# Kernel optimization log

Measured on AMD Instinct MI355X. Metric: run time of the kernel, lower is better.

Reference implementation:

```python
import jax, jax.numpy as jnp
import numpy as np

TEMPERATURE = 0.07
ALPHA = 1.0
GAMMA = 2.0
EPS = 1e-12  # F.normalize eps


def _l2_normalize(x):
    # matches F.normalize: x / max(||x||_2, eps)
    norm = jnp.sqrt(jnp.sum(x * x, axis=-1, keepdims=True))
    return x / jnp.maximum(norm, EPS)


def setup_inputs() -> dict:
    key = jax.random.key(0)
    k1, k2 = jax.random.split(key)
    B, D = 8192, 64
    image_features = jax.random.normal(k1, (B, D), dtype=jnp.float32)
    text_features = jax.random.normal(k2, (B, D), dtype=jnp.float32)
    return {"image_features": image_features, "text_features": text_features}


def reference(image_features, text_features):
    img = _l2_normalize(image_features)
    txt = _l2_normalize(text_features)
    logits = jnp.einsum("bd,cd->bc", img, txt) / TEMPERATURE  # [B, B]
    B = logits.shape[0]
    idx = jnp.arange(B)

    logp_row = jax.nn.log_softmax(logits, axis=-1)  # i2t CE source
    logp_col = jax.nn.log_softmax(logits, axis=0)   # t2i CE source

    diag_logp_row = logp_row[idx, idx]
    diag_logp_col = logp_col[idx, idx]

    # focal weight uses ROW-softmax positive prob for BOTH directions (as in source)
    p_pos = jnp.exp(diag_logp_row)
    w = ALPHA * (1.0 - p_pos) ** GAMMA

    focal_i2t = jnp.mean(w * (-diag_logp_row))
    focal_t2i = jnp.mean(w * (-diag_logp_col))
    return (focal_i2t + focal_t2i) / 2.0
```

## Files before the change

### kernel.cpp

```cpp
#include <hip/hip_runtime.h>
#include <hip/hip_bf16.h>


#define NB 8192
#define ND 64

constexpr float INV_T = 1.0f / 0.07f;
constexpr float LOG2E = 1.4426950408889634f;
constexpr float LN2   = 0.6931471805599453f;
constexpr float K1    = INV_T * LOG2E;

typedef float  floatx4 __attribute__((ext_vector_type(4)));
typedef short  bf16x8  __attribute__((ext_vector_type(8)));
typedef short  shortx4 __attribute__((ext_vector_type(4)));

__global__ __launch_bounds__(256)
void norm_kernel(const float* __restrict__ img, const float* __restrict__ txt,
                 __hip_bfloat16* __restrict__ imgB,
                 __hip_bfloat16* __restrict__ txtB,
                 float* __restrict__ diag,
                 float* __restrict__ out)
{
    if (blockIdx.x == 0 && threadIdx.x == 0) out[0] = 0.f;

    const int lane = threadIdx.x & 63;
    const int gw   = blockIdx.x * 4 + (threadIdx.x >> 6);
    const int sub  = lane >> 4;
    const int c16  = lane & 15;
    const int row  = gw * 4 + sub;

    const floatx4 x = ((const floatx4*)img)[row * 16 + c16];
    const floatx4 t = ((const floatx4*)txt)[row * 16 + c16];
    float sx  = x[0]*x[0] + x[1]*x[1] + x[2]*x[2] + x[3]*x[3];
    float st  = t[0]*t[0] + t[1]*t[1] + t[2]*t[2] + t[3]*t[3];
    float sxt = x[0]*t[0] + x[1]*t[1] + x[2]*t[2] + x[3]*t[3];
    #pragma unroll
    for (int o = 1; o < 16; o <<= 1) {
        sx  += __shfl_xor(sx,  o, 64);
        st  += __shfl_xor(st,  o, 64);
        sxt += __shfl_xor(sxt, o, 64);
    }
    const float nx = fmaxf(sqrtf(sx), 1e-12f);
    const float nt = fmaxf(sqrtf(st), 1e-12f);
    shortx4 xb, tb;
    #pragma unroll
    for (int j = 0; j < 4; ++j) {
        __hip_bfloat16 hx = __float2bfloat16(x[j] / nx * K1);
        __hip_bfloat16 ht = __float2bfloat16(t[j] / nt);
        xb[j] = *reinterpret_cast<const short*>(&hx);
        tb[j] = *reinterpret_cast<const short*>(&ht);
    }
    ((shortx4*)imgB)[row * 16 + c16] = xb;
    ((shortx4*)txtB)[row * 16 + c16] = tb;
    if (c16 == 0) diag[row] = sxt / (nx * nt) * INV_T;
}

__global__ __launch_bounds__(256)
void score_kernel(const __hip_bfloat16* __restrict__ imgB,
                  const __hip_bfloat16* __restrict__ txtB,
                  float* __restrict__ rowPart,
                  float* __restrict__ colPart)
{
    const int wid   = threadIdx.x >> 6;
    const int lane  = threadIdx.x & 63;
    const int chunk = blockIdx.x & 31;
    const int sgrp  = blockIdx.x >> 5;
    const int strip = sgrp * 4 + wid;
    const int m = lane & 15;
    const int q = lane >> 4;

    __shared__ float sm[4][256];

    const bf16x8* __restrict__ A  = (const bf16x8*)imgB;
    const bf16x8* __restrict__ Bp = (const bf16x8*)txtB;

    const int rowbase = strip * 64;
    bf16x8 a[4][2];
    #pragma unroll
    for (int it = 0; it < 4; ++it) {
        const int r = rowbase + it * 16 + m;
        a[it][0] = A[r * 8 + q];
        a[it][1] = A[r * 8 + 4 + q];
    }

    const int colbase = chunk * 256 + m;
    bf16x8 b0 = Bp[colbase * 8 + q];
    bf16x8 b1 = Bp[colbase * 8 + 4 + q];

    float rs[16];
    #pragma unroll
    for (int i = 0; i < 16; ++i) rs[i] = 0.f;

    const floatx4 NEGK = {-K1, -K1, -K1, -K1};

    #pragma unroll 2
    for (int t = 0; t < 16; ++t) {
        const int nn = colbase + (((t + 1) & 15) << 4);
        const bf16x8 pb0 = Bp[nn * 8 + q];
        const bf16x8 pb1 = Bp[nn * 8 + 4 + q];

        float csp[4];
        #pragma unroll
        for (int it = 0; it < 4; ++it) {
            floatx4 z   = __builtin_amdgcn_mfma_f32_16x16x32_bf16(a[it][0], b0, NEGK, 0, 0, 0);
            floatx4 acc = __builtin_amdgcn_mfma_f32_16x16x32_bf16(a[it][1], b1, z,    0, 0, 0);
            const float e0 = __builtin_amdgcn_exp2f(acc[0]);
            const float e1 = __builtin_amdgcn_exp2f(acc[1]);
            const float e2 = __builtin_amdgcn_exp2f(acc[2]);
            const float e3 = __builtin_amdgcn_exp2f(acc[3]);
            rs[it * 4 + 0] += e0;
            rs[it * 4 + 1] += e1;
            rs[it * 4 + 2] += e2;
            rs[it * 4 + 3] += e3;
            csp[it] = (e0 + e1) + (e2 + e3);
        }
        float cs = (csp[0] + csp[1]) + (csp[2] + csp[3]);
        cs += __shfl_xor(cs, 16, 64);
        cs += __shfl_xor(cs, 32, 64);
        if (q == 0) sm[wid][(t << 4) + m] = cs;
        b0 = pb0; b1 = pb1;
    }

#define RS_STAGE(d)                                                     \
    {                                                                   \
        const bool hi = (m & (d)) != 0;                                 \
        _Pragma("unroll")                                               \
        for (int j = 0; j < (d); ++j) {                                 \
            const float va = rs[j], vb = rs[j + (d)];                   \
            const float send = hi ? va : vb;                            \
            const float recv = __shfl_xor(send, (d), 64);               \
            rs[j] = (hi ? vb : va) + recv;                              \
        }                                                               \
    }
    RS_STAGE(8)
    RS_STAGE(4)
    RS_STAGE(2)
    RS_STAGE(1)
#undef RS_STAGE

    const int row = rowbase + ((m >> 2) << 4) + (q << 2) + (m & 3);
    rowPart[chunk * NB + row] = rs[0];

    __syncthreads();
    const int j = threadIdx.x;
    const float v = (sm[0][j] + sm[1][j]) + (sm[2][j] + sm[3][j]);
    colPart[sgrp * NB + chunk * 256 + j] = v;
}

__global__ __launch_bounds__(256)
void finish_kernel(const float* __restrict__ rowPart,
                   const float* __restrict__ colPart,
                   const float* __restrict__ diag,
                   float* __restrict__ out)
{
    const int tg = blockIdx.x * 256 + threadIdx.x;
    const int i  = tg >> 3;
    const int p  = threadIdx.x & 7;

    float rowS = 0.f, colS = 0.f;
    #pragma unroll
    for (int u = 0; u < 4; ++u) {
        rowS += rowPart[(p * 4 + u) * NB + i];
        colS += colPart[(p * 4 + u) * NB + i];
    }
    #pragma unroll
    for (int o = 1; o < 8; o <<= 1) {
        rowS += __shfl_xor(rowS, o, 64);
        colS += __shfl_xor(colS, o, 64);
    }

    float contrib = 0.f;
    if (p == 0) {
        const float d     = diag[i];
        const float lse_r = INV_T + __builtin_amdgcn_logf(rowS) * LN2;
        const float lse_c = INV_T + __builtin_amdgcn_logf(colS) * LN2;
        const float lpr = d - lse_r;
        const float lpc = d - lse_c;
        const float pp  = __builtin_amdgcn_exp2f(lpr * LOG2E);
        const float om  = 1.f - pp;
        contrib = om * om * (-lpr - lpc) * (0.5f / (float)NB);
    }
    #pragma unroll
    for (int o = 8; o < 64; o <<= 1) contrib += __shfl_xor(contrib, o, 64);

    __shared__ float red[4];
    if ((threadIdx.x & 63) == 0) red[threadIdx.x >> 6] = contrib;
    __syncthreads();
    if (threadIdx.x == 0)
        atomicAdd(out, red[0] + red[1] + red[2] + red[3]);
}

extern "C" void kernel_launch(void* const* d_in, const int* in_sizes, int n_in,
                              void* d_out, int out_size, void* d_ws, size_t ws_size,
                              hipStream_t stream)
{
    const float* img = (const float*)d_in[0];
    const float* txt = (const float*)d_in[1];

    char* ws = (char*)d_ws;
    __hip_bfloat16* imgB = (__hip_bfloat16*)(ws);
    __hip_bfloat16* txtB = (__hip_bfloat16*)(ws + (1u << 20));
    float* diag    = (float*)(ws + (2u << 20));
    float* rowPart = (float*)(ws + (2u << 20) + (1u << 15));
    float* colPart = (float*)(ws + (3u << 20) + (1u << 15));

    norm_kernel<<<512, 256, 0, stream>>>(img, txt, imgB, txtB, diag, (float*)d_out);
    score_kernel<<<1024, 256, 0, stream>>>(imgB, txtB, rowPart, colPart);
    finish_kernel<<<256, 256, 0, stream>>>(rowPart, colPart, diag, (float*)d_out);
}
```

Measured before the change: 84.71 us.

## Fuse norm, score and finish into one cooperative kernel with grid syncs

Merges the three launches into a single cooperative kernel of 1024 blocks that uses grid.sync() between the normalize, score and reduction phases. The finish phase is re-split so each of the 1024 blocks handles 8 rows, with 32 lanes per row. The aim is to remove the launch gaps and tail effects between kernels. The cost is two grid-wide barriers and a requirement that all 1024 blocks are co-resident (launch bounds 256,4); if the cooperative launch fails, the code falls back to the original three-kernel path.

```diff
diff --git a/kernel.cpp b/kernel.cpp
--- a/kernel.cpp
+++ b/kernel.cpp
@@ -1,5 +1,8 @@
 #include <hip/hip_runtime.h>
 #include <hip/hip_bf16.h>
+#include <hip/hip_cooperative_groups.h>
+
+namespace cg = cooperative_groups;
 
 
 #define NB 8192
@@ -14,20 +17,16 @@
 typedef short  bf16x8  __attribute__((ext_vector_type(8)));
 typedef short  shortx4 __attribute__((ext_vector_type(4)));
 
-__global__ __launch_bounds__(256)
-void norm_kernel(const float* __restrict__ img, const float* __restrict__ txt,
-                 __hip_bfloat16* __restrict__ imgB,
-                 __hip_bfloat16* __restrict__ txtB,
-                 float* __restrict__ diag,
-                 float* __restrict__ out)
-{
-    if (blockIdx.x == 0 && threadIdx.x == 0) out[0] = 0.f;
-
-    const int lane = threadIdx.x & 63;
-    const int gw   = blockIdx.x * 4 + (threadIdx.x >> 6);
-    const int sub  = lane >> 4;
-    const int c16  = lane & 15;
-    const int row  = gw * 4 + sub;
+__device__ __forceinline__
+void norm_body(int gw, int lane,
+               const float* __restrict__ img, const float* __restrict__ txt,
+               __hip_bfloat16* __restrict__ imgB,
+               __hip_bfloat16* __restrict__ txtB,
+               float* __restrict__ diag)
+{
+    const int sub = lane >> 4;
+    const int c16 = lane & 15;
+    const int row = gw * 4 + sub;
 
     const floatx4 x = ((const floatx4*)img)[row * 16 + c16];
     const floatx4 t = ((const floatx4*)txt)[row * 16 + c16];
@@ -55,21 +54,18 @@
     if (c16 == 0) diag[row] = sxt / (nx * nt) * INV_T;
 }
 
-__global__ __launch_bounds__(256)
-void score_kernel(const __hip_bfloat16* __restrict__ imgB,
-                  const __hip_bfloat16* __restrict__ txtB,
-                  float* __restrict__ rowPart,
-                  float* __restrict__ colPart)
-{
-    const int wid   = threadIdx.x >> 6;
-    const int lane  = threadIdx.x & 63;
-    const int chunk = blockIdx.x & 31;
-    const int sgrp  = blockIdx.x >> 5;
+__device__ __forceinline__
+void score_body(int bid, int wid, int lane, float (*sm)[256],
+                const __hip_bfloat16* __restrict__ imgB,
+                const __hip_bfloat16* __restrict__ txtB,
+                float* __restrict__ rowPart,
+                float* __restrict__ colPart)
+{
+    const int chunk = bid & 31;
+    const int sgrp  = bid >> 5;
     const int strip = sgrp * 4 + wid;
     const int m = lane & 15;
     const int q = lane >> 4;
-
-    __shared__ float sm[4][256];
 
     const bf16x8* __restrict__ A  = (const bf16x8*)imgB;
     const bf16x8* __restrict__ Bp = (const bf16x8*)txtB;
@@ -147,6 +143,86 @@
     colPart[sgrp * NB + chunk * 256 + j] = v;
 }
 
+__global__ __launch_bounds__(256, 4)
+void fused_kernel(const float* __restrict__ img, const float* __restrict__ txt,
+                  __hip_bfloat16* __restrict__ imgB,
+                  __hip_bfloat16* __restrict__ txtB,
+                  float* __restrict__ diag,
+                  float* __restrict__ rowPart,
+                  float* __restrict__ colPart,
+                  float* __restrict__ out)
+{
+    cg::grid_group grid = cg::this_grid();
+    const int wid  = threadIdx.x >> 6;
+    const int lane = threadIdx.x & 63;
+
+    __shared__ float sm[4][256];
+
+    if (blockIdx.x == 0 && threadIdx.x == 0) out[0] = 0.f;
+    if (blockIdx.x < 512)
+        norm_body(blockIdx.x * 4 + wid, lane, img, txt, imgB, txtB, diag);
+
+    grid.sync();
+
+    score_body(blockIdx.x, wid, lane, sm, imgB, txtB, rowPart, colPart);
+
+    grid.sync();
+
+    {
+        const int tg = blockIdx.x * 256 + threadIdx.x;
+        const int i  = tg >> 5;
+        const int p  = threadIdx.x & 31;
+
+        float rowS = rowPart[p * NB + i];
+        float colS = colPart[p * NB + i];
+        #pragma unroll
+        for (int o = 1; o < 32; o <<= 1) {
+            rowS += __shfl_xor(rowS, o, 64);
+            colS += __shfl_xor(colS, o, 64);
+        }
+
+        float contrib = 0.f;
+        if (p == 0) {
+            const float d     = diag[i];
+            const float lse_r = INV_T + __builtin_amdgcn_logf(rowS) * LN2;
+            const float lse_c = INV_T + __builtin_amdgcn_logf(colS) * LN2;
+            const float lpr = d - lse_r;
+            const float lpc = d - lse_c;
+            const float pp  = __builtin_amdgcn_exp2f(lpr * LOG2E);
+            const float om  = 1.f - pp;
+            contrib = om * om * (-lpr - lpc) * (0.5f / (float)NB);
+        }
+        contrib += __shfl_xor(contrib, 32, 64);
+
+        __shared__ float red[4];
+        if (lane == 0) red[wid] = contrib;
+        __syncthreads();
+        if (threadIdx.x == 0)
+            atomicAdd(out, red[0] + red[1] + red[2] + red[3]);
+    }
+}
+
+__global__ __launch_bounds__(256)
+void norm_kernel(const float* __restrict__ img, const float* __restrict__ txt,
+                 __hip_bfloat16* __restrict__ imgB,
+                 __hip_bfloat16* __restrict__ txtB,
+                 float* __restrict__ diag, float* __restrict__ out)
+{
+    if (blockIdx.x == 0 && threadIdx.x == 0) out[0] = 0.f;
+    norm_body(blockIdx.x * 4 + (threadIdx.x >> 6), threadIdx.x & 63,
+              img, txt, imgB, txtB, diag);
+}
+
+__global__ __launch_bounds__(256)
+void score_kernel(const __hip_bfloat16* __restrict__ imgB,
+                  const __hip_bfloat16* __restrict__ txtB,
+                  float* __restrict__ rowPart, float* __restrict__ colPart)
+{
+    __shared__ float sm[4][256];
+    score_body(blockIdx.x, threadIdx.x >> 6, threadIdx.x & 63, sm,
+               imgB, txtB, rowPart, colPart);
+}
+
 __global__ __launch_bounds__(256)
 void finish_kernel(const float* __restrict__ rowPart,
                    const float* __restrict__ colPart,
@@ -156,7 +232,6 @@
     const int tg = blockIdx.x * 256 + threadIdx.x;
     const int i  = tg >> 3;
     const int p  = threadIdx.x & 7;
-
     float rowS = 0.f, colS = 0.f;
     #pragma unroll
     for (int u = 0; u < 4; ++u) {
@@ -168,7 +243,6 @@
         rowS += __shfl_xor(rowS, o, 64);
         colS += __shfl_xor(colS, o, 64);
     }
-
     float contrib = 0.f;
     if (p == 0) {
         const float d     = diag[i];
@@ -182,7 +256,6 @@
     }
     #pragma unroll
     for (int o = 8; o < 64; o <<= 1) contrib += __shfl_xor(contrib, o, 64);
-
     __shared__ float red[4];
     if ((threadIdx.x & 63) == 0) red[threadIdx.x >> 6] = contrib;
     __syncthreads();
@@ -203,8 +276,16 @@
     float* diag    = (float*)(ws + (2u << 20));
     float* rowPart = (float*)(ws + (2u << 20) + (1u << 15));
     float* colPart = (float*)(ws + (3u << 20) + (1u << 15));
-
-    norm_kernel<<<512, 256, 0, stream>>>(img, txt, imgB, txtB, diag, (float*)d_out);
-    score_kernel<<<1024, 256, 0, stream>>>(imgB, txtB, rowPart, colPart);
-    finish_kernel<<<256, 256, 0, stream>>>(rowPart, colPart, diag, (float*)d_out);
-}
+    float* outp    = (float*)d_out;
+
+    void* args[] = {(void*)&img, (void*)&txt, (void*)&imgB, (void*)&txtB,
+                    (void*)&diag, (void*)&rowPart, (void*)&colPart, (void*)&outp};
+    hipError_t err = hipLaunchCooperativeKernel((void*)fused_kernel,
+                                                dim3(1024), dim3(256),
+                                                args, 0, stream);
+    if (err != hipSuccess) {
+        norm_kernel<<<512, 256, 0, stream>>>(img, txt, imgB, txtB, diag, outp);
+        score_kernel<<<1024, 256, 0, stream>>>(imgB, txtB, rowPart, colPart);
+        finish_kernel<<<256, 256, 0, stream>>>(rowPart, colPart, diag, outp);
+    }
+}
```

Measured after the change: 257.8 us. +204.4%, slower.

## Fuse finish reduction into score kernel via last-blocks atomic counter

Applied to the files above, without the earlier changes.

Removes the separate finish kernel launch. Each score block bumps a global counter once its partial sums are written, and the last 32 blocks to arrive spin until every block is done, then each reduces 256 rows of partials into the loss. This saves one launch and its gap but serializes the final reduction onto 32 blocks that must wait for the slowest block. The spin-wait only avoids deadlock because the waiting blocks take the final ranks, after every other block has already started.

```diff
diff --git a/kernel.cpp b/kernel.cpp
--- a/kernel.cpp
+++ b/kernel.cpp
@@ -4,6 +4,9 @@
 
 #define NB 8192
 #define ND 64
+#define NBLK 1024
+#define NFIN 32
+#define FIN_START (NBLK - NFIN)
 
 constexpr float INV_T = 1.0f / 0.07f;
 constexpr float LOG2E = 1.4426950408889634f;
@@ -19,9 +22,10 @@
                  __hip_bfloat16* __restrict__ imgB,
                  __hip_bfloat16* __restrict__ txtB,
                  float* __restrict__ diag,
+                 int* __restrict__ counter,
                  float* __restrict__ out)
 {
-    if (blockIdx.x == 0 && threadIdx.x == 0) out[0] = 0.f;
+    if (blockIdx.x == 0 && threadIdx.x == 0) { out[0] = 0.f; *counter = 0; }
 
     const int lane = threadIdx.x & 63;
     const int gw   = blockIdx.x * 4 + (threadIdx.x >> 6);
@@ -56,10 +60,13 @@
 }
 
 __global__ __launch_bounds__(256)
-void score_kernel(const __hip_bfloat16* __restrict__ imgB,
-                  const __hip_bfloat16* __restrict__ txtB,
-                  float* __restrict__ rowPart,
-                  float* __restrict__ colPart)
+void score_finish_kernel(const __hip_bfloat16* __restrict__ imgB,
+                         const __hip_bfloat16* __restrict__ txtB,
+                         float* __restrict__ rowPart,
+                         float* __restrict__ colPart,
+                         const float* __restrict__ diag,
+                         int* __restrict__ counter,
+                         float* __restrict__ out)
 {
     const int wid   = threadIdx.x >> 6;
     const int lane  = threadIdx.x & 63;
@@ -142,49 +149,53 @@
     rowPart[chunk * NB + row] = rs[0];
 
     __syncthreads();
-    const int j = threadIdx.x;
-    const float v = (sm[0][j] + sm[1][j]) + (sm[2][j] + sm[3][j]);
-    colPart[sgrp * NB + chunk * 256 + j] = v;
-}
-
-__global__ __launch_bounds__(256)
-void finish_kernel(const float* __restrict__ rowPart,
-                   const float* __restrict__ colPart,
-                   const float* __restrict__ diag,
-                   float* __restrict__ out)
-{
-    const int tg = blockIdx.x * 256 + threadIdx.x;
-    const int i  = tg >> 3;
-    const int p  = threadIdx.x & 7;
-
+    {
+        const int j = threadIdx.x;
+        const float v = (sm[0][j] + sm[1][j]) + (sm[2][j] + sm[3][j]);
+        colPart[sgrp * NB + chunk * 256 + j] = v;
+    }
+
+    __shared__ int s_rank;
+    __threadfence();
+    __syncthreads();
+    if (threadIdx.x == 0) {
+        const int r = atomicAdd(counter, 1);
+        s_rank = r;
+        if (r >= FIN_START) {
+            while (__hip_atomic_load(counter, __ATOMIC_RELAXED,
+                                     __HIP_MEMORY_SCOPE_AGENT) < NBLK)
+                __builtin_amdgcn_s_sleep(8);
+        }
+    }
+    __syncthreads();
+    const int rank = s_rank;
+    if (rank < FIN_START) return;
+    __threadfence();
+
+    const int i = (rank - FIN_START) * 256 + threadIdx.x;
     float rowS = 0.f, colS = 0.f;
-    #pragma unroll
-    for (int u = 0; u < 4; ++u) {
-        rowS += rowPart[(p * 4 + u) * NB + i];
-        colS += colPart[(p * 4 + u) * NB + i];
-    }
-    #pragma unroll
-    for (int o = 1; o < 8; o <<= 1) {
-        rowS += __shfl_xor(rowS, o, 64);
-        colS += __shfl_xor(colS, o, 64);
-    }
-
-    float contrib = 0.f;
-    if (p == 0) {
-        const float d     = diag[i];
-        const float lse_r = INV_T + __builtin_amdgcn_logf(rowS) * LN2;
-        const float lse_c = INV_T + __builtin_amdgcn_logf(colS) * LN2;
-        const float lpr = d - lse_r;
-        const float lpc = d - lse_c;
-        const float pp  = __builtin_amdgcn_exp2f(lpr * LOG2E);
-        const float om  = 1.f - pp;
-        contrib = om * om * (-lpr - lpc) * (0.5f / (float)NB);
-    }
-    #pragma unroll
-    for (int o = 8; o < 64; o <<= 1) contrib += __shfl_xor(contrib, o, 64);
-
+    #pragma unroll 8
+    for (int c = 0; c < 32; ++c)
+        rowS += __hip_atomic_load(&rowPart[c * NB + i], __ATOMIC_RELAXED,
+                                  __HIP_MEMORY_SCOPE_AGENT);
+    #pragma unroll 8
+    for (int c = 0; c < 32; ++c)
+        colS += __hip_atomic_load(&colPart[c * NB + i], __ATOMIC_RELAXED,
+                                  __HIP_MEMORY_SCOPE_AGENT);
+
+    const float d     = diag[i];
+    const float lse_r = INV_T + __builtin_amdgcn_logf(rowS) * LN2;
+    const float lse_c = INV_T + __builtin_amdgcn_logf(colS) * LN2;
+    const float lpr = d - lse_r;
+    const float lpc = d - lse_c;
+    const float pp  = __builtin_amdgcn_exp2f(lpr * LOG2E);
+    const float om  = 1.f - pp;
+    float contrib = om * om * (-lpr - lpc) * (0.5f / (float)NB);
+
+    #pragma unroll
+    for (int o = 1; o < 64; o <<= 1) contrib += __shfl_xor(contrib, o, 64);
     __shared__ float red[4];
-    if ((threadIdx.x & 63) == 0) red[threadIdx.x >> 6] = contrib;
+    if (lane == 0) red[wid] = contrib;
     __syncthreads();
     if (threadIdx.x == 0)
         atomicAdd(out, red[0] + red[1] + red[2] + red[3]);
@@ -203,8 +214,10 @@
     float* diag    = (float*)(ws + (2u << 20));
     float* rowPart = (float*)(ws + (2u << 20) + (1u << 15));
     float* colPart = (float*)(ws + (3u << 20) + (1u << 15));
-
-    norm_kernel<<<512, 256, 0, stream>>>(img, txt, imgB, txtB, diag, (float*)d_out);
-    score_kernel<<<1024, 256, 0, stream>>>(imgB, txtB, rowPart, colPart);
-    finish_kernel<<<256, 256, 0, stream>>>(rowPart, colPart, diag, (float*)d_out);
+    int*   counter = (int*)  (ws + (4u << 20) + (1u << 15));
+    float* outp    = (float*)d_out;
+
+    norm_kernel<<<512, 256, 0, stream>>>(img, txt, imgB, txtB, diag, counter, outp);
+    score_finish_kernel<<<NBLK, 256, 0, stream>>>(imgB, txtB, rowPart, colPart,
+                                                  diag, counter, outp);
 }
```

Measured after the change: 161.6 us. 1.91x slower.
